# Kernel tuning notes

Hardware: AMD Instinct MI355X
Metric: run time of the kernel (lower is better)

Reference implementation:

```python
import math
import jax, jax.numpy as jnp
from jax import lax
import numpy as np

D_MODEL = 2048
N_HEADS = 16
HEAD_DIM = 128
INNER = N_HEADS * HEAD_DIM  # 2048
KCONV = 4
B, N = 2, 2048


def setup_inputs() -> dict:
    key = jax.random.key(0)
    ks = jax.random.split(key, 7)
    x = jax.random.normal(ks[0], (B, N, D_MODEL), dtype=jnp.float32)
    W_qkv = jax.random.normal(ks[1], (3 * INNER, D_MODEL), dtype=jnp.float32) * 0.02
    conv_w = jax.random.normal(ks[2], (3 * INNER, KCONV), dtype=jnp.float32) * 0.2
    W_ab = jax.random.normal(ks[3], (2 * N_HEADS, D_MODEL), dtype=jnp.float32) * 0.02
    # ab_proj bias init: first H filled with log(0.98/0.02), rest zero
    b_ab = jnp.concatenate([
        jnp.full((N_HEADS,), math.log(0.98 / 0.02), dtype=jnp.float32),
        jnp.zeros((N_HEADS,), dtype=jnp.float32),
    ])
    W_g = jax.random.normal(ks[4], (INNER, D_MODEL), dtype=jnp.float32) * 0.02
    W_o = jax.random.normal(ks[5], (D_MODEL, INNER), dtype=jnp.float32) * 0.02
    return {"x": x, "W_qkv": W_qkv, "conv_w": conv_w, "W_ab": W_ab,
            "b_ab": b_ab, "W_g": W_g, "W_o": W_o}


def _l2_normalize(t, eps=1e-12):
    # torch F.normalize: x / max(||x||_2, eps)
    nrm = jnp.sqrt(jnp.sum(t * t, axis=-1, keepdims=True))
    return t / jnp.maximum(nrm, eps)


def _short_conv(z, conv_w):
    # depthwise causal conv1d + SiLU (FLA-style ShortConvolution, no bias)
    # z: (B, N, C), conv_w: (C, K)
    C, K = conv_w.shape
    zc = jnp.transpose(z, (0, 2, 1))  # (B, C, N)
    kern = conv_w[:, None, :]          # (C, 1, K) -> OIH
    out = lax.conv_general_dilated(
        zc, kern, window_strides=(1,), padding=[(K - 1, 0)],
        dimension_numbers=("NCH", "OIH", "NCH"), feature_group_count=C)
    return jax.nn.silu(jnp.transpose(out, (0, 2, 1)))  # (B, N, C)


def reference(x, W_qkv, conv_w, W_ab, b_ab, W_g, W_o):
    Bq, Nq, _ = x.shape
    H = b_ab.shape[0] // 2
    inner = W_g.shape[0]
    D = inner // H

    qkv = jnp.einsum("bnd,ed->bne", x, W_qkv)            # (B, N, 3*inner)
    qkv = _short_conv(qkv, conv_w)
    q, k, v = jnp.split(qkv, 3, axis=-1)
    to_heads = lambda t: t.reshape(Bq, Nq, H, D).transpose(0, 2, 1, 3)  # (B,H,N,D)
    q, k, v = to_heads(q), to_heads(k), to_heads(v)
    q = _l2_normalize(q)
    k = _l2_normalize(k)

    ab = jnp.einsum("bnd,ed->bne", x, W_ab) + b_ab        # (B, N, 2H)
    alpha = jax.nn.sigmoid(ab[..., :H]).transpose(0, 2, 1)  # (B, H, N)
    beta = jax.nn.sigmoid(ab[..., H:]).transpose(0, 2, 1)   # (B, H, N)

    # gated delta rule recurrence:
    #   S_t = a_t * S_{t-1} + b_t * (v_t - a_t * S_{t-1} k_t) k_t^T
    #   o_t = S_t q_t
    # time-major xs for scan
    q_s = q.transpose(2, 0, 1, 3)   # (N, B, H, D)
    k_s = k.transpose(2, 0, 1, 3)
    v_s = v.transpose(2, 0, 1, 3)
    a_s = alpha.transpose(2, 0, 1)  # (N, B, H)
    b_s = beta.transpose(2, 0, 1)

    S0 = jnp.zeros((Bq, H, D, D), dtype=x.dtype)

    def step(S, inp):
        q_t, k_t, v_t, a_t, b_t = inp
        Sk = jnp.einsum("bhde,bhe->bhd", S, k_t)
        u = b_t[..., None] * (v_t - a_t[..., None] * Sk)
        S = a_t[..., None, None] * S + u[..., :, None] * k_t[..., None, :]
        o = jnp.einsum("bhde,bhe->bhd", S, q_t)
        return S, o

    _, o = lax.scan(step, S0, (q_s, k_s, v_s, a_s, b_s))  # o: (N, B, H, D)
    out = o.transpose(1, 0, 2, 3).reshape(Bq, Nq, inner)

    g = jax.nn.silu(jnp.einsum("bnd,ed->bne", x, W_g))
    out = out * g
    y = jnp.einsum("bne,de->bnd", out, W_o)
    return y
```

## Files before the change

kernel.cpp:

```cpp
#include <hip/hip_runtime.h>
#include <math.h>
#include <stddef.h>

#define B_ 2
#define N_ 2048
#define DM 2048
#define H_ 16
#define HD 128
#define INNER 2048
#define TRIPLE 6144
#define M_ (B_ * N_)
#define T_ 32
#define NCHK (N_ / T_)

typedef __bf16 bf16x8 __attribute__((ext_vector_type(8)));
typedef float  f32x4v __attribute__((ext_vector_type(4)));
typedef __attribute__((address_space(1))) const void gvoid;
typedef __attribute__((address_space(3))) void lvoid;

__device__ __forceinline__ float sig_(float x) { return 1.0f / (1.0f + __expf(-x)); }

__device__ __forceinline__ unsigned short f2bf(float f) {
    unsigned u = __float_as_uint(f);
    u += 0x7FFFu + ((u >> 16) & 1u);
    return (unsigned short)(u >> 16);
}
__device__ __forceinline__ float bf2f(unsigned short h) {
    return __uint_as_float((unsigned)h << 16);
}
__device__ __forceinline__ void unpack8(uint4 r, float* f) {
    f[0] = __uint_as_float(r.x << 16); f[1] = __uint_as_float(r.x & 0xffff0000u);
    f[2] = __uint_as_float(r.y << 16); f[3] = __uint_as_float(r.y & 0xffff0000u);
    f[4] = __uint_as_float(r.z << 16); f[5] = __uint_as_float(r.z & 0xffff0000u);
    f[6] = __uint_as_float(r.w << 16); f[7] = __uint_as_float(r.w & 0xffff0000u);
}

__device__ __forceinline__ void lds_barrier() {
    asm volatile("" ::: "memory");
    __builtin_amdgcn_s_waitcnt(0xC07F);
    __builtin_amdgcn_s_barrier();
    asm volatile("" ::: "memory");
}

__device__ __forceinline__ void bar() {
    asm volatile("" ::: "memory");
    __builtin_amdgcn_s_barrier();
    asm volatile("" ::: "memory");
}

__global__ __launch_bounds__(256) void cast_bf16_3(
    const float* __restrict__ s1, const float* __restrict__ s2,
    const float* __restrict__ s3, unsigned short* __restrict__ dst,
    int n1, int n2, int n3)
{
    int i = (blockIdx.x * 256 + threadIdx.x) * 4;
    const float* s; int off;
    if (i < n1)           { s = s1; off = i; }
    else if (i < n1 + n2) { s = s2; off = i - n1; }
    else if (i < n1 + n2 + n3) { s = s3; off = i - n1 - n2; }
    else return;
    float4 v = *(const float4*)(s + off);
    ushort4 u;
    u.x = f2bf(v.x); u.y = f2bf(v.y); u.z = f2bf(v.z); u.w = f2bf(v.w);
    *(ushort4*)(dst + i) = u;
}

__global__ __launch_bounds__(256) void cast_hilo(
    const float* __restrict__ in, unsigned short* __restrict__ hi,
    unsigned short* __restrict__ lo, int n)
{
    int i = (blockIdx.x * 256 + threadIdx.x) * 4;
    if (i < n) {
        float4 v = *(const float4*)(in + i);
        ushort4 h, l;
        h.x = f2bf(v.x); l.x = f2bf(v.x - bf2f(h.x));
        h.y = f2bf(v.y); l.y = f2bf(v.y - bf2f(h.y));
        h.z = f2bf(v.z); l.z = f2bf(v.z - bf2f(h.z));
        h.w = f2bf(v.w); l.w = f2bf(v.w - bf2f(h.w));
        *(ushort4*)(hi + i) = h;
        *(ushort4*)(lo + i) = l;
    }
}

__global__ __launch_bounds__(512) void gemm_fused256(
    const unsigned short* __restrict__ A, const unsigned short* __restrict__ Bw,
    unsigned short* __restrict__ outQ, float* __restrict__ outG,
    int M, int NQ, int NG, int K)
{
    __shared__ unsigned short As[2][256 * 64];
    __shared__ unsigned short Bs[2][256 * 64];

    const int tid = threadIdx.x;
    const int w   = tid >> 6;
    const int l   = tid & 63;
    const int wm  = w >> 2;
    const int wn  = w & 3;
    const int lr  = l & 15;
    const int kg  = l >> 4;

    const int bid = blockIdx.x;
    const int swz = (bid & 7) * 64 + (bid >> 3);
    const int by  = swz & 15;
    const int bx  = swz >> 4;
    const int row0 = by * 256;
    const int col0 = bx * 256;

    const int srow = w * 8 + (l >> 3);
    const int schk = ((l & 7) ^ (l >> 3)) * 8;
    const unsigned short* Ath = A  + (size_t)(row0 + srow) * K + schk;
    const unsigned short* Bth = Bw + (size_t)(col0 + srow) * K + schk;

    const int fsw0 = ((0 + kg) ^ (lr & 7)) * 8;
    const int fsw1 = ((4 + kg) ^ (lr & 7)) * 8;
    const int arb  = wm * 64 + lr;
    const int brb  = wn * 32 + lr;

    f32x4v acc[2][2][4][2];
#pragma unroll
    for (int a0 = 0; a0 < 2; ++a0)
#pragma unroll
        for (int a1 = 0; a1 < 2; ++a1)
#pragma unroll
            for (int a2 = 0; a2 < 4; ++a2)
#pragma unroll
                for (int a3 = 0; a3 < 2; ++a3)
                    acc[a0][a1][a2][a3] = (f32x4v){0.f, 0.f, 0.f, 0.f};

#define STAGE_A(b, hb, kt) do {                                                  \
        const unsigned short* g_ = Ath + (size_t)((hb) * 128) * K + (kt) * 64;   \
        unsigned short* d_ = &As[b][((hb) * 128 + w * 8) * 64];                  \
        __builtin_amdgcn_global_load_lds((gvoid*)g_, (lvoid*)d_, 16, 0, 0);      \
        __builtin_amdgcn_global_load_lds((gvoid*)(g_ + (size_t)64 * K),          \
                                         (lvoid*)(d_ + 64 * 64), 16, 0, 0);      \
    } while (0)
#define STAGE_B(b, hb, kt) do {                                                  \
        const unsigned short* g_ = Bth + (size_t)((hb) * 128) * K + (kt) * 64;   \
        unsigned short* d_ = &Bs[b][((hb) * 128 + w * 8) * 64];                  \
        __builtin_amdgcn_global_load_lds((gvoid*)g_, (lvoid*)d_, 16, 0, 0);      \
        __builtin_amdgcn_global_load_lds((gvoid*)(g_ + (size_t)64 * K),          \
                                         (lvoid*)(d_ + 64 * 64), 16, 0, 0);      \
    } while (0)

#define RD_A(DST, BASE, HOFF)                                        \
    _Pragma("unroll")                                                \
    for (int m_ = 0; m_ < 4; ++m_) {                                 \
        const int r_ = ((HOFF) + arb + m_ * 16) * 64;                \
        DST[m_][0] = *(const bf16x8*)((BASE) + r_ + fsw0);           \
        DST[m_][1] = *(const bf16x8*)((BASE) + r_ + fsw1);           \
    }
#define RD_B(DST, BASE, HOFF)                                        \
    _Pragma("unroll")                                                \
    for (int n_ = 0; n_ < 2; ++n_) {                                 \
        const int r_ = ((HOFF) + brb + n_ * 16) * 64;                \
        DST[n_][0] = *(const bf16x8*)((BASE) + r_ + fsw0);           \
        DST[n_][1] = *(const bf16x8*)((BASE) + r_ + fsw1);           \
    }
#define Q_MFMA(MH, NH, AF, BF)                                               \
    __builtin_amdgcn_s_setprio(1);                                           \
    _Pragma("unroll")                                                        \
    for (int m_ = 0; m_ < 4; ++m_)                                           \
        _Pragma("unroll")                                                    \
        for (int n_ = 0; n_ < 2; ++n_) {                                     \
            acc[MH][NH][m_][n_] = __builtin_amdgcn_mfma_f32_16x16x32_bf16(   \
                AF[m_][0], BF[n_][0], acc[MH][NH][m_][n_], 0, 0, 0);         \
            acc[MH][NH][m_][n_] = __builtin_amdgcn_mfma_f32_16x16x32_bf16(   \
                AF[m_][1], BF[n_][1], acc[MH][NH][m_][n_], 0, 0, 0);         \
        }                                                                    \
    __builtin_amdgcn_s_setprio(0);

    const int KT = K >> 6;

    STAGE_A(0, 0, 0); STAGE_B(0, 0, 0); STAGE_A(0, 1, 0); STAGE_B(0, 1, 0);
    STAGE_A(1, 0, 1); STAGE_B(1, 1, 1);
    asm volatile("s_waitcnt vmcnt(4)" ::: "memory");
    bar();

    bf16x8 aF[4][2];
    bf16x8 aG[4][2];
    bf16x8 bF0[2][2];
    bf16x8 bF1[2][2];

#pragma unroll 2
    for (int kt = 0; kt < KT; ++kt) {
        const unsigned short* Ab = As[kt & 1];
        const unsigned short* Bb = Bs[kt & 1];
        const int nb = (kt + 1) & 1;

        RD_A(aF, Ab, 0);
        RD_B(bF0, Bb, 0);
        if (kt + 1 < KT) STAGE_B(nb, 0, kt + 1);
        bar();

        Q_MFMA(0, 0, aF, bF0);
        RD_B(bF1, Bb, 128);
        if (kt + 1 < KT) STAGE_A(nb, 1, kt + 1);
        bar();

        Q_MFMA(0, 1, aF, bF1);
        RD_A(aG, Ab, 128);
        if (kt + 2 < KT) STAGE_A(kt & 1, 0, kt + 2);
        bar();

        Q_MFMA(1, 1, aG, bF1);
        if (kt + 2 < KT) STAGE_B(kt & 1, 1, kt + 2);
        if (kt < KT - 2)       { asm volatile("s_waitcnt vmcnt(4)" ::: "memory"); }
        else if (kt == KT - 2) { asm volatile("s_waitcnt vmcnt(0)" ::: "memory"); }
        bar();
        Q_MFMA(1, 0, aG, bF0);
    }
#undef STAGE_A
#undef STAGE_B
#undef RD_A
#undef RD_B
#undef Q_MFMA

    const bool isG = (col0 >= NQ);
#pragma unroll
    for (int mh = 0; mh < 2; ++mh)
#pragma unroll
    for (int m = 0; m < 4; ++m) {
        const int rbase = row0 + mh * 128 + wm * 64 + m * 16 + kg * 4;
#pragma unroll
        for (int nh = 0; nh < 2; ++nh)
#pragma unroll
        for (int n = 0; n < 2; ++n) {
            const int c = col0 + nh * 128 + wn * 32 + n * 16 + lr;
#pragma unroll
            for (int j = 0; j < 4; ++j) {
                float v = acc[mh][nh][m][n][j];
                const size_t r = (size_t)(rbase + j);
                if (!isG) {
                    outQ[r * NQ + c] = f2bf(v);
                } else {
                    v = v * sig_(v);
                    outG[r * NG + (c - NQ)] = v;
                }
            }
        }
    }
}

__global__ __launch_bounds__(256) void gemm_bf16f(
    const unsigned short* __restrict__ A, const unsigned short* __restrict__ Bw,
    float* __restrict__ C, int M, int N, int K)
{
    __shared__ unsigned short As[2][128 * 64];
    __shared__ unsigned short Bs[2][128 * 64];

    const int tid = threadIdx.x;
    const int w   = tid >> 6;
    const int l   = tid & 63;
    const int wm  = w >> 1;
    const int wn  = w & 1;
    const int lr  = l & 15;
    const int kg  = l >> 4;

    const int bid = blockIdx.x;
    const int swz = (bid & 7) * 64 + (bid >> 3);
    const int by  = swz & 31;
    const int bx  = swz >> 5;
    const int row0 = by * 128;
    const int col0 = bx * 128;

    const int srow = w * 8 + (l >> 3);
    const int schk = ((l & 7) ^ (l >> 3)) * 8;
    const unsigned short* Ath = A  + (size_t)(row0 + srow) * K + schk;
    const unsigned short* Bth = Bw + (size_t)(col0 + srow) * K + schk;

    const int fsw0 = ((0 + kg) ^ (lr & 7)) * 8;
    const int fsw1 = ((4 + kg) ^ (lr & 7)) * 8;
    const int arb  = wm * 64 + lr;
    const int brb  = wn * 64 + lr;

    f32x4v acc[4][4];
#pragma unroll
    for (int i = 0; i < 4; ++i)
#pragma unroll
        for (int j = 0; j < 4; ++j) acc[i][j] = (f32x4v){0.f, 0.f, 0.f, 0.f};

#define STAGE_T(buf, kt) do {                                                    \
        _Pragma("unroll")                                                        \
        for (int p_ = 0; p_ < 4; ++p_) {                                         \
            const unsigned short* ga_ = Ath + (size_t)(p_ * 32) * K + (kt) * 64; \
            const unsigned short* gb_ = Bth + (size_t)(p_ * 32) * K + (kt) * 64; \
            unsigned short* da_ = &As[buf][(p_ * 32 + w * 8) * 64];              \
            unsigned short* db_ = &Bs[buf][(p_ * 32 + w * 8) * 64];              \
            __builtin_amdgcn_global_load_lds((gvoid*)ga_, (lvoid*)da_, 16, 0, 0);\
            __builtin_amdgcn_global_load_lds((gvoid*)gb_, (lvoid*)db_, 16, 0, 0);\
        }                                                                        \
    } while (0)

    const int KT = K >> 6;

    STAGE_T(0, 0);
    STAGE_T(1, 1);
    asm volatile("s_waitcnt vmcnt(8)" ::: "memory");
    bar();

    bf16x8 aF[4][2], bF[4][2];

#pragma unroll 2
    for (int kt = 0; kt < KT; ++kt) {
        const unsigned short* Ab = As[kt & 1];
        const unsigned short* Bb = Bs[kt & 1];

#pragma unroll
        for (int m_ = 0; m_ < 4; ++m_) {
            const int r_ = (arb + m_ * 16) * 64;
            aF[m_][0] = *(const bf16x8*)(Ab + r_ + fsw0);
            aF[m_][1] = *(const bf16x8*)(Ab + r_ + fsw1);
        }
#pragma unroll
        for (int n_ = 0; n_ < 4; ++n_) {
            const int r_ = (brb + n_ * 16) * 64;
            bF[n_][0] = *(const bf16x8*)(Bb + r_ + fsw0);
            bF[n_][1] = *(const bf16x8*)(Bb + r_ + fsw1);
        }
        bar();

        if (kt + 2 < KT) STAGE_T(kt & 1, kt + 2);

        __builtin_amdgcn_s_setprio(1);
#pragma unroll
        for (int ks = 0; ks < 2; ++ks)
#pragma unroll
            for (int m_ = 0; m_ < 4; ++m_)
#pragma unroll
                for (int n_ = 0; n_ < 4; ++n_)
                    acc[m_][n_] = __builtin_amdgcn_mfma_f32_16x16x32_bf16(
                        aF[m_][ks], bF[n_][ks], acc[m_][n_], 0, 0, 0);
        __builtin_amdgcn_s_setprio(0);

        if (kt < KT - 2) {
            asm volatile("s_waitcnt vmcnt(8)" ::: "memory");
        } else if (kt == KT - 2) {
            asm volatile("s_waitcnt vmcnt(0)" ::: "memory");
        }
        bar();
    }
#undef STAGE_T

#pragma unroll
    for (int m_ = 0; m_ < 4; ++m_)
#pragma unroll
        for (int j = 0; j < 4; ++j) {
            const int r = row0 + wm * 64 + m_ * 16 + kg * 4 + j;
#pragma unroll
            for (int n_ = 0; n_ < 4; ++n_) {
                const int c = col0 + wn * 64 + n_ * 16 + lr;
                C[(size_t)r * N + c] = acc[m_][n_][j];
            }
        }
}

__global__ __launch_bounds__(256) void gemm_ab(
    const unsigned short* __restrict__ xhi, const unsigned short* __restrict__ xlo,
    const unsigned short* __restrict__ wh, const unsigned short* __restrict__ wl,
    const float* __restrict__ b_ab, float* __restrict__ absig)
{
    __shared__ float sums[4][16][32];
    const int tid = threadIdx.x;
    const int w = tid >> 6, lane = tid & 63;
    const int lr = lane & 15, lk8 = (lane >> 4) * 8, lrow4 = (lane >> 4) * 4;
    const int row = blockIdx.x * 16 + lr;
    const int kw  = w * (DM / 4);

    f32x4v acc[2];
    acc[0] = (f32x4v){0.f,0.f,0.f,0.f};
    acc[1] = (f32x4v){0.f,0.f,0.f,0.f};
    const unsigned short* Ah = xhi + (size_t)row * DM + kw;
    const unsigned short* Al = xlo + (size_t)row * DM + kw;

    for (int k0 = 0; k0 < DM / 4; k0 += 32) {
        bf16x8 ah = *(const bf16x8*)(Ah + k0 + lk8);
        bf16x8 al = *(const bf16x8*)(Al + k0 + lk8);
#pragma unroll
        for (int nt = 0; nt < 2; ++nt) {
            bf16x8 whf = *(const bf16x8*)(wh + (size_t)(nt * 16 + lr) * DM + kw + k0 + lk8);
            bf16x8 wlf = *(const bf16x8*)(wl + (size_t)(nt * 16 + lr) * DM + kw + k0 + lk8);
            acc[nt] = __builtin_amdgcn_mfma_f32_16x16x32_bf16(ah, whf, acc[nt], 0, 0, 0);
            acc[nt] = __builtin_amdgcn_mfma_f32_16x16x32_bf16(ah, wlf, acc[nt], 0, 0, 0);
            acc[nt] = __builtin_amdgcn_mfma_f32_16x16x32_bf16(al, whf, acc[nt], 0, 0, 0);
        }
    }

#pragma unroll
    for (int nt = 0; nt < 2; ++nt)
#pragma unroll
        for (int j = 0; j < 4; ++j)
            sums[w][lrow4 + j][nt * 16 + lr] = acc[nt][j];
    __syncthreads();

// ... 210 lines not shown
        const size_t cb = (size_t)bh * NCHK;
        const unsigned short* Am = Ab + (size_t)(mt * 16 + lr) * TRIPLE;
#pragma unroll
        for (int ks = 0; ks < 4; ++ks) aF[ks] = *(const bf16x8*)(Am + ks * 32 + lk8);
        if (!isQ) {
            wmF = *(const bf16x8*)(What + cb * (T_*T_) + (mt * 16 + lr) * T_ + lk8);
#pragma unroll
            for (int j = 0; j < 4; ++j)
                sc4[j] = Ubar[cb * (T_*HD) + (mt * 16 + lrow4 + j) * HD + d0 + lr];
        } else {
            wmF = *(const bf16x8*)(Mhat + cb * (T_*T_) + (mt * 16 + lr) * T_ + lk8);
#pragma unroll
            for (int j = 0; j < 4; ++j) {
                sc4[j] = Pbuf[cb * T_ + mt * 16 + lrow4 + j];
                g4[j]  = gb[(size_t)(mt * 16 + lrow4 + j) * INNER + d0 + lr];
            }
        }
#pragma unroll
        for (int j2 = 0; j2 < 2; ++j2)
            khF[j2] = *(const bf16x8*)(KhatT + cb * (HD*T_) + ((2*w + j2) * 16 + lr) * T_ + lk8);
        gam = Pbuf[cb * T_ + T_ - 1];
    }
    __syncthreads();

    for (int c = 0; c < NCHK; ++c) {
        const int np = (c + 1 < NCHK) ? c + 1 : c;
        const size_t cbn = (size_t)bh * NCHK + np;
        const int tok0n = np * T_;
        bf16x8 aFn[4], wmFn, khFn[2];
        float sc4n[4], g4n[4], gamn;
        {
            const unsigned short* Am = Ab + (size_t)(tok0n + mt * 16 + lr) * TRIPLE;
#pragma unroll
            for (int ks = 0; ks < 4; ++ks) aFn[ks] = *(const bf16x8*)(Am + ks * 32 + lk8);
            if (!isQ) {
                wmFn = *(const bf16x8*)(What + cbn * (T_*T_) + (mt * 16 + lr) * T_ + lk8);
#pragma unroll
                for (int j = 0; j < 4; ++j)
                    sc4n[j] = Ubar[cbn * (T_*HD) + (mt * 16 + lrow4 + j) * HD + d0 + lr];
            } else {
                wmFn = *(const bf16x8*)(Mhat + cbn * (T_*T_) + (mt * 16 + lr) * T_ + lk8);
#pragma unroll
                for (int j = 0; j < 4; ++j) {
                    sc4n[j] = Pbuf[cbn * T_ + mt * 16 + lrow4 + j];
                    g4n[j]  = gb[(size_t)(tok0n + mt * 16 + lrow4 + j) * INNER + d0 + lr];
                }
            }
#pragma unroll
            for (int j2 = 0; j2 < 2; ++j2)
                khFn[j2] = *(const bf16x8*)(KhatT + cbn * (HD*T_) + ((2*w + j2) * 16 + lr) * T_ + lk8);
            gamn = Pbuf[cbn * T_ + T_ - 1];
        }

        f32x4v accH = {0.f,0.f,0.f,0.f}, accL = {0.f,0.f,0.f,0.f};
#pragma unroll
        for (int ks = 0; ks < 4; ++ks) {
            bf16x8 hi = *(const bf16x8*)&Shi[lr * 136 + ks * 32 + lk8];
            bf16x8 lo = *(const bf16x8*)&Slo[lr * 136 + ks * 32 + lk8];
            accH = __builtin_amdgcn_mfma_f32_16x16x32_bf16(aF[ks], hi, accH, 0, 0, 0);
            accL = __builtin_amdgcn_mfma_f32_16x16x32_bf16(aF[ks], lo, accL, 0, 0, 0);
        }
        f32x4v accB;
#pragma unroll
        for (int j = 0; j < 4; ++j) accB[j] = accH[j] + accL[j];

        if (!isQ) {
            ushort4 cv;
            cv.x = f2bf(-accB[0]); cv.y = f2bf(-accB[1]);
            cv.z = f2bf(-accB[2]); cv.w = f2bf(-accB[3]);
            *(ushort4*)&CT[lr * 40 + mt * 16 + lrow4] = cv;
        }
        lds_barrier();

        if (!isQ) {
            f32x4v accU;
#pragma unroll
            for (int j = 0; j < 4; ++j) accU[j] = sc4[j];
            bf16x8 bC = *(const bf16x8*)&CT[lr * 40 + lk8];
            accU = __builtin_amdgcn_mfma_f32_16x16x32_bf16(wmF, bC, accU, 0, 0, 0);
            ushort4 uv;
            uv.x = f2bf(accU[0]); uv.y = f2bf(accU[1]);
            uv.z = f2bf(accU[2]); uv.w = f2bf(accU[3]);
            *(ushort4*)&UT[lr * 40 + mt * 16 + lrow4] = uv;
        }
        lds_barrier();

        bf16x8 utF = *(const bf16x8*)&UT[lr * 40 + lk8];

        if (isQ) {
            f32x4v accO;
#pragma unroll
            for (int j = 0; j < 4; ++j) accO[j] = sc4[j] * accB[j];
            accO = __builtin_amdgcn_mfma_f32_16x16x32_bf16(wmF, utF, accO, 0, 0, 0);
            const int tokb = c * T_ + mt * 16 + lrow4;
#pragma unroll
            for (int j = 0; j < 4; ++j)
                ogb[(size_t)(tokb + j) * INNER + d0 + lr] = f2bf(accO[j] * g4[j]);
        }

#pragma unroll
        for (int j2 = 0; j2 < 2; ++j2) {
            const int et = 2 * w + j2;
            f32x4v accS;
#pragma unroll
            for (int j = 0; j < 4; ++j)
                accS[j] = gam * S[(lrow4 + j) * 132 + et * 16 + lr];
            accS = __builtin_amdgcn_mfma_f32_16x16x32_bf16(utF, khF[j2], accS, 0, 0, 0);
#pragma unroll
            for (int j = 0; j < 4; ++j) {
                float v = accS[j];
                S[(lrow4 + j) * 132 + et * 16 + lr] = v;
                unsigned short hh = f2bf(v);
                Shi[(lrow4 + j) * 136 + et * 16 + lr] = hh;
                Slo[(lrow4 + j) * 136 + et * 16 + lr] = f2bf(v - bf2f(hh));
            }
        }
        lds_barrier();

#pragma unroll
        for (int ks = 0; ks < 4; ++ks) aF[ks] = aFn[ks];
        wmF = wmFn;
#pragma unroll
        for (int j = 0; j < 4; ++j) { sc4[j] = sc4n[j]; g4[j] = g4n[j]; }
        khF[0] = khFn[0]; khF[1] = khFn[1];
        gam = gamn;
    }
}

extern "C" void kernel_launch(void* const* d_in, const int* in_sizes, int n_in,
                              void* d_out, int out_size, void* d_ws, size_t ws_size,
                              hipStream_t stream) {
    const float* x      = (const float*)d_in[0];
    const float* W_qkv  = (const float*)d_in[1];
    const float* conv_w = (const float*)d_in[2];
    const float* W_ab   = (const float*)d_in[3];
    const float* b_ab   = (const float*)d_in[4];
    const float* W_g    = (const float*)d_in[5];
    const float* W_o    = (const float*)d_in[6];
    float* out = (float*)d_out;

    char* p = (char*)d_ws;
    unsigned short* wqkvb   = (unsigned short*)p; p += (size_t)TRIPLE * DM * 2;
    unsigned short* wgb     = (unsigned short*)p; p += (size_t)INNER * DM * 2;
    unsigned short* wob     = (unsigned short*)p; p += (size_t)DM * INNER * 2;
    unsigned short* wabhi   = (unsigned short*)p; p += (size_t)32 * DM * 2;
    unsigned short* wablo   = (unsigned short*)p; p += (size_t)32 * DM * 2;
    unsigned short* xb      = (unsigned short*)p; p += (size_t)M_ * DM * 2;
    unsigned short* xlo     = (unsigned short*)p; p += (size_t)M_ * DM * 2;
    unsigned short* qkv_pre = (unsigned short*)p; p += (size_t)M_ * TRIPLE * 2;
    unsigned short* qkv_c   = (unsigned short*)p; p += (size_t)M_ * TRIPLE * 2;
    float*          absig   = (float*)p;          p += (size_t)M_ * 32 * 4;
    float*          gpre    = (float*)p;          p += (size_t)M_ * INNER * 4;
    unsigned short* ogb     = (unsigned short*)p; p += (size_t)M_ * INNER * 2;

    char* q = (char*)xb;
    float*          Ubar  = (float*)q;          q += (size_t)32 * NCHK * T_ * HD * 4;
    unsigned short* KhatT = (unsigned short*)q; q += (size_t)32 * NCHK * HD * T_ * 2;
    unsigned short* What  = (unsigned short*)q; q += (size_t)32 * NCHK * T_ * T_ * 2;
    unsigned short* Mhat  = (unsigned short*)q; q += (size_t)32 * NCHK * T_ * T_ * 2;
    float*          Pbuf  = (float*)q;          q += (size_t)32 * NCHK * T_ * 4;

    dim3 blk(256);
    cast_hilo<<<dim3((M_ * DM) / 1024), blk, 0, stream>>>(x, xb, xlo, M_ * DM);
    cast_bf16_3<<<dim3((TRIPLE * DM + INNER * DM + DM * INNER) / 1024), blk, 0, stream>>>(
        W_qkv, W_g, W_o, wqkvb, TRIPLE * DM, INNER * DM, DM * INNER);
    cast_hilo<<<dim3((32 * DM) / 1024), blk, 0, stream>>>(W_ab, wabhi, wablo, 32 * DM);

    gemm_fused256<<<dim3(((TRIPLE + INNER) / 256) * (M_ / 256)), dim3(512), 0, stream>>>(
        xb, wqkvb, qkv_pre, gpre, M_, TRIPLE, INNER, DM);
    gemm_ab<<<dim3(M_ / 16), blk, 0, stream>>>(xb, xlo, wabhi, wablo, b_ab, absig);
    conv_silu_norm<<<dim3(B_ * N_), blk, 0, stream>>>(qkv_pre, conv_w, qkv_c);

    chunk_prep<<<dim3(32 * NCHK), blk, 0, stream>>>(qkv_c, absig, Ubar, What, Mhat, KhatT, Pbuf);
    chunk_scan<<<dim3(256), blk, 0, stream>>>(qkv_c, gpre, Ubar, What, Mhat, KhatT, Pbuf, ogb);

    gemm_bf16f<<<dim3((M_ / 128) * (INNER / 128)), blk, 0, stream>>>(
        ogb, wob, out, M_, INNER, DM);
}
```

Measured before the change: 556.1 us.

## Pre-pack weights into MFMA fragment layout and load B directly to registers

The QKV+gate weights are cast to bf16 in a packed layout of 16x32 fragments, so each lane of the fused GEMM can load its B operand straight from global memory into registers with contiguous 16-byte reads. This removes the B tile from LDS, which halves shared memory use and drops two of the four barriers per k-tile. The main loop is rewritten as a register double-buffered two-step body, with A still staged through LDS. It trades LDS traffic and syncs for more global load latency on the critical path and extra register pressure. The W_o cast becomes a separate kernel with scalar stores.

```diff
diff --git a/kernel.cpp b/kernel.cpp
--- a/kernel.cpp
+++ b/kernel.cpp
@@ -48,21 +48,35 @@
     asm volatile("" ::: "memory");
 }
 
-__global__ __launch_bounds__(256) void cast_bf16_3(
-    const float* __restrict__ s1, const float* __restrict__ s2,
-    const float* __restrict__ s3, unsigned short* __restrict__ dst,
-    int n1, int n2, int n3)
+__global__ __launch_bounds__(256) void cast_bf16(
+    const float* __restrict__ in, unsigned short* __restrict__ out, int n)
 {
     int i = (blockIdx.x * 256 + threadIdx.x) * 4;
-    const float* s; int off;
-    if (i < n1)           { s = s1; off = i; }
-    else if (i < n1 + n2) { s = s2; off = i - n1; }
-    else if (i < n1 + n2 + n3) { s = s3; off = i - n1 - n2; }
-    else return;
-    float4 v = *(const float4*)(s + off);
-    ushort4 u;
-    u.x = f2bf(v.x); u.y = f2bf(v.y); u.z = f2bf(v.z); u.w = f2bf(v.w);
-    *(ushort4*)(dst + i) = u;
+    if (i < n) {
+        float4 v = *(const float4*)(in + i);
+        out[i + 0] = f2bf(v.x); out[i + 1] = f2bf(v.y);
+        out[i + 2] = f2bf(v.z); out[i + 3] = f2bf(v.w);
+    }
+}
+
+__global__ __launch_bounds__(256) void pack_cast_w(
+    const float* __restrict__ Wq, const float* __restrict__ Wg,
+    unsigned short* __restrict__ dst)
+{
+    const int i = blockIdx.x * 256 + threadIdx.x;
+    const int e = i * 8;
+    const int n = e >> 11;
+    const int k = e & 2047;
+    const float* src = (n < TRIPLE) ? (Wq + (size_t)n * DM + k)
+                                    : (Wg + (size_t)(n - TRIPLE) * DM + k);
+    float4 v0 = *(const float4*)(src);
+    float4 v1 = *(const float4*)(src + 4);
+    ushort4 u0, u1;
+    u0.x = f2bf(v0.x); u0.y = f2bf(v0.y); u0.z = f2bf(v0.z); u0.w = f2bf(v0.w);
+    u1.x = f2bf(v1.x); u1.y = f2bf(v1.y); u1.z = f2bf(v1.z); u1.w = f2bf(v1.w);
+    const size_t off = ((size_t)((n >> 4) * 64 + (k >> 5)) << 9) + (n & 15) * 32 + (k & 31);
+    *(ushort4*)(dst + off)     = u0;
+    *(ushort4*)(dst + off + 4) = u1;
 }
 
 __global__ __launch_bounds__(256) void cast_hilo(
@@ -83,12 +97,11 @@
 }
 
 __global__ __launch_bounds__(512) void gemm_fused256(
-    const unsigned short* __restrict__ A, const unsigned short* __restrict__ Bw,
+    const unsigned short* __restrict__ A, const unsigned short* __restrict__ Bp,
     unsigned short* __restrict__ outQ, float* __restrict__ outG,
     int M, int NQ, int NG, int K)
 {
     __shared__ unsigned short As[2][256 * 64];
-    __shared__ unsigned short Bs[2][256 * 64];
 
     const int tid = threadIdx.x;
     const int w   = tid >> 6;
@@ -107,13 +120,19 @@
 
     const int srow = w * 8 + (l >> 3);
     const int schk = ((l & 7) ^ (l >> 3)) * 8;
-    const unsigned short* Ath = A  + (size_t)(row0 + srow) * K + schk;
-    const unsigned short* Bth = Bw + (size_t)(col0 + srow) * K + schk;
+    const unsigned short* Ath = A + (size_t)(row0 + srow) * K + schk;
 
     const int fsw0 = ((0 + kg) ^ (lr & 7)) * 8;
     const int fsw1 = ((4 + kg) ^ (lr & 7)) * 8;
     const int arb  = wm * 64 + lr;
-    const int brb  = wn * 32 + lr;
+
+    const unsigned short* Bl0 = Bp + lr * 32 + kg * 8;
+    int nbOff[2][2];
+#pragma unroll
+    for (int nh_ = 0; nh_ < 2; ++nh_)
+#pragma unroll
+        for (int n_ = 0; n_ < 2; ++n_)
+            nbOff[nh_][n_] = (((col0 >> 4) + nh_ * 8 + wn * 2 + n_) << 15);
 
     f32x4v acc[2][2][4][2];
 #pragma unroll
@@ -126,19 +145,24 @@
                 for (int a3 = 0; a3 < 2; ++a3)
                     acc[a0][a1][a2][a3] = (f32x4v){0.f, 0.f, 0.f, 0.f};
 
-#define STAGE_A(b, hb, kt) do {                                                  \
-        const unsigned short* g_ = Ath + (size_t)((hb) * 128) * K + (kt) * 64;   \
-        unsigned short* d_ = &As[b][((hb) * 128 + w * 8) * 64];                  \
-        __builtin_amdgcn_global_load_lds((gvoid*)g_, (lvoid*)d_, 16, 0, 0);      \
-        __builtin_amdgcn_global_load_lds((gvoid*)(g_ + (size_t)64 * K),          \
-                                         (lvoid*)(d_ + 64 * 64), 16, 0, 0);      \
+#define STAGE_T(buf, kt) do {                                                    \
+        _Pragma("unroll")                                                        \
+        for (int p_ = 0; p_ < 4; ++p_) {                                         \
+            const unsigned short* g_ = Ath + (size_t)(p_ * 64) * K + (kt) * 64;  \
+            unsigned short* d_ = &As[buf][(p_ * 64 + w * 8) * 64];               \
+            __builtin_amdgcn_global_load_lds((gvoid*)g_, (lvoid*)d_, 16, 0, 0);  \
+        }                                                                        \
     } while (0)
-#define STAGE_B(b, hb, kt) do {                                                  \
-        const unsigned short* g_ = Bth + (size_t)((hb) * 128) * K + (kt) * 64;   \
-        unsigned short* d_ = &Bs[b][((hb) * 128 + w * 8) * 64];                  \
-        __builtin_amdgcn_global_load_lds((gvoid*)g_, (lvoid*)d_, 16, 0, 0);      \
-        __builtin_amdgcn_global_load_lds((gvoid*)(g_ + (size_t)64 * K),          \
-                                         (lvoid*)(d_ + 64 * 64), 16, 0, 0);      \
+
+#define LOAD_B(DST, kt) do {                                                     \
+        _Pragma("unroll")                                                        \
+        for (int nh_ = 0; nh_ < 2; ++nh_)                                        \
+        _Pragma("unroll")                                                        \
+        for (int n_ = 0; n_ < 2; ++n_)                                           \
+        _Pragma("unroll")                                                        \
+        for (int ks_ = 0; ks_ < 2; ++ks_)                                        \
+            DST[nh_][n_][ks_] = *(const bf16x8*)(                                \
+                Bl0 + nbOff[nh_][n_] + ((kt) * 2 + ks_) * 512);                  \
     } while (0)
 
 #define RD_A(DST, BASE, HOFF)                                        \
@@ -148,70 +172,59 @@
         DST[m_][0] = *(const bf16x8*)((BASE) + r_ + fsw0);           \
         DST[m_][1] = *(const bf16x8*)((BASE) + r_ + fsw1);           \
     }
-#define RD_B(DST, BASE, HOFF)                                        \
-    _Pragma("unroll")                                                \
-    for (int n_ = 0; n_ < 2; ++n_) {                                 \
-        const int r_ = ((HOFF) + brb + n_ * 16) * 64;                \
-        DST[n_][0] = *(const bf16x8*)((BASE) + r_ + fsw0);           \
-        DST[n_][1] = *(const bf16x8*)((BASE) + r_ + fsw1);           \
-    }
-#define Q_MFMA(MH, NH, AF, BF)                                               \
+
+#define Q_MFMA(MH, NH, AF, BB)                                               \
     __builtin_amdgcn_s_setprio(1);                                           \
     _Pragma("unroll")                                                        \
     for (int m_ = 0; m_ < 4; ++m_)                                           \
         _Pragma("unroll")                                                    \
         for (int n_ = 0; n_ < 2; ++n_) {                                     \
             acc[MH][NH][m_][n_] = __builtin_amdgcn_mfma_f32_16x16x32_bf16(   \
-                AF[m_][0], BF[n_][0], acc[MH][NH][m_][n_], 0, 0, 0);         \
+                AF[m_][0], BB[NH][n_][0], acc[MH][NH][m_][n_], 0, 0, 0);     \
             acc[MH][NH][m_][n_] = __builtin_amdgcn_mfma_f32_16x16x32_bf16(   \
-                AF[m_][1], BF[n_][1], acc[MH][NH][m_][n_], 0, 0, 0);         \
+                AF[m_][1], BB[NH][n_][1], acc[MH][NH][m_][n_], 0, 0, 0);     \
         }                                                                    \
     __builtin_amdgcn_s_setprio(0);
 
     const int KT = K >> 6;
 
-    STAGE_A(0, 0, 0); STAGE_B(0, 0, 0); STAGE_A(0, 1, 0); STAGE_B(0, 1, 0);
-    STAGE_A(1, 0, 1); STAGE_B(1, 1, 1);
-    asm volatile("s_waitcnt vmcnt(4)" ::: "memory");
+    bf16x8 aF[4][2], aG[4][2];
+    bf16x8 bX[2][2][2], bY[2][2][2];
+
+    STAGE_T(0, 0);
+    STAGE_T(1, 1);
+    LOAD_B(bX, 0);
+    asm volatile("s_waitcnt vmcnt(12)" ::: "memory");
     bar();
 
-    bf16x8 aF[4][2];
-    bf16x8 aG[4][2];
-    bf16x8 bF0[2][2];
-    bf16x8 bF1[2][2];
-
-#pragma unroll 2
-    for (int kt = 0; kt < KT; ++kt) {
-        const unsigned short* Ab = As[kt & 1];
-        const unsigned short* Bb = Bs[kt & 1];
-        const int nb = (kt + 1) & 1;
-
-        RD_A(aF, Ab, 0);
-        RD_B(bF0, Bb, 0);
-        if (kt + 1 < KT) STAGE_B(nb, 0, kt + 1);
-        bar();
-
-        Q_MFMA(0, 0, aF, bF0);
-        RD_B(bF1, Bb, 128);
-        if (kt + 1 < KT) STAGE_A(nb, 1, kt + 1);
-        bar();
-
-        Q_MFMA(0, 1, aF, bF1);
-        RD_A(aG, Ab, 128);
-        if (kt + 2 < KT) STAGE_A(kt & 1, 0, kt + 2);
-        bar();
-
-        Q_MFMA(1, 1, aG, bF1);
-        if (kt + 2 < KT) STAGE_B(kt & 1, 1, kt + 2);
-        if (kt < KT - 2)       { asm volatile("s_waitcnt vmcnt(4)" ::: "memory"); }
-        else if (kt == KT - 2) { asm volatile("s_waitcnt vmcnt(0)" ::: "memory"); }
-        bar();
-        Q_MFMA(1, 0, aG, bF0);
-    }
-#undef STAGE_A
-#undef STAGE_B
+#define TILE_BODY(kt, BCUR, BNXT) do {                                          \
+        const unsigned short* Ab = As[(kt) & 1];                                \
+        RD_A(aF, Ab, 0);                                                        \
+        if ((kt) + 1 < KT) LOAD_B(BNXT, (kt) + 1);                              \
+        Q_MFMA(0, 0, aF, BCUR);                                                 \
+        Q_MFMA(0, 1, aF, BCUR);                                                 \
+        RD_A(aG, Ab, 128);                                                      \
+        Q_MFMA(1, 1, aG, BCUR);                                                 \
+        Q_MFMA(1, 0, aG, BCUR);                                                 \
+        if ((kt) + 2 < KT) {                                                    \
+            bar();                             \
+            STAGE_T((kt) & 1, (kt) + 2);                                        \
+        }                                                                       \
+        if ((kt) + 1 < KT) {                                                    \
+            if ((kt) < KT - 2) { asm volatile("s_waitcnt vmcnt(12)" ::: "memory"); } \
+            else               { asm volatile("s_waitcnt vmcnt(8)"  ::: "memory"); } \
+            bar();                                  \
+        }                                                                       \
+    } while (0)
+
+    for (int kt = 0; kt < KT; kt += 2) {
+        TILE_BODY(kt,     bX, bY);
+        TILE_BODY(kt + 1, bY, bX);
+    }
+#undef TILE_BODY
+#undef STAGE_T
+#undef LOAD_B
 #undef RD_A
-#undef RD_B
 #undef Q_MFMA
 
     const bool isG = (col0 >= NQ);
@@ -754,6 +767,7 @@
     float*          absig   = (float*)p;          p += (size_t)M_ * 32 * 4;
     float*          gpre    = (float*)p;          p += (size_t)M_ * INNER * 4;
     unsigned short* ogb     = (unsigned short*)p; p += (size_t)M_ * INNER * 2;
+    (void)wgb;
 
     char* q = (char*)xb;
     float*          Ubar  = (float*)q;          q += (size_t)32 * NCHK * T_ * HD * 4;
@@ -764,8 +778,9 @@
 
     dim3 blk(256);
     cast_hilo<<<dim3((M_ * DM) / 1024), blk, 0, stream>>>(x, xb, xlo, M_ * DM);
-    cast_bf16_3<<<dim3((TRIPLE * DM + INNER * DM + DM * INNER) / 1024), blk, 0, stream>>>(
-        W_qkv, W_g, W_o, wqkvb, TRIPLE * DM, INNER * DM, DM * INNER);
+    pack_cast_w<<<dim3(((TRIPLE + INNER) * DM / 8) / 256), blk, 0, stream>>>(
+        W_qkv, W_g, wqkvb);
+    cast_bf16<<<dim3((INNER * DM) / 1024), blk, 0, stream>>>(W_o, wob, INNER * DM);
     cast_hilo<<<dim3((32 * DM) / 1024), blk, 0, stream>>>(W_ab, wabhi, wablo, 32 * DM);
 
     gemm_fused256<<<dim3(((TRIPLE + INNER) / 256) * (M_ / 256)), dim3(512), 0, stream>>>(
```

Result: slower. 585.0 us (+5.2%).

## Switch fused QKV/gate GEMM to 128x128 tiles and merge cast kernels

Applied to the files above, without the earlier changes.

Replaces the 256x256, 512-thread fused projection GEMM with a 128x128, 256-thread version that uses a simpler two-stage global-to-LDS double buffer. This gives four times as many blocks and less LDS per block, and folds the three fp32-to-bf16 cast launches into one kernel. The aim is better occupancy and load balance across CUs and fewer launches. In exchange, each block reuses less data, which raises global/L2 traffic per FLOP.

```diff
diff --git a/kernel.cpp b/kernel.cpp
--- a/kernel.cpp
+++ b/kernel.cpp
@@ -48,62 +48,72 @@
     asm volatile("" ::: "memory");
 }
 
-__global__ __launch_bounds__(256) void cast_bf16_3(
-    const float* __restrict__ s1, const float* __restrict__ s2,
-    const float* __restrict__ s3, unsigned short* __restrict__ dst,
-    int n1, int n2, int n3)
+#define NX_ (M_ * DM)
+#define NW_ ((TRIPLE + 2 * INNER) * DM)
+#define NAB_ (32 * DM)
+__global__ __launch_bounds__(256) void cast_all(
+    const float* __restrict__ x, const float* __restrict__ Wq,
+    const float* __restrict__ Wg, const float* __restrict__ Wo,
+    const float* __restrict__ Wab,
+    unsigned short* __restrict__ xb, unsigned short* __restrict__ xlo,
+    unsigned short* __restrict__ wfused,
+    unsigned short* __restrict__ wabhi, unsigned short* __restrict__ wablo)
 {
-    int i = (blockIdx.x * 256 + threadIdx.x) * 4;
-    const float* s; int off;
-    if (i < n1)           { s = s1; off = i; }
-    else if (i < n1 + n2) { s = s2; off = i - n1; }
-    else if (i < n1 + n2 + n3) { s = s3; off = i - n1 - n2; }
-    else return;
-    float4 v = *(const float4*)(s + off);
-    ushort4 u;
-    u.x = f2bf(v.x); u.y = f2bf(v.y); u.z = f2bf(v.z); u.w = f2bf(v.w);
-    *(ushort4*)(dst + i) = u;
-}
-
-__global__ __launch_bounds__(256) void cast_hilo(
-    const float* __restrict__ in, unsigned short* __restrict__ hi,
-    unsigned short* __restrict__ lo, int n)
-{
-    int i = (blockIdx.x * 256 + threadIdx.x) * 4;
-    if (i < n) {
-        float4 v = *(const float4*)(in + i);
+    const int i = (blockIdx.x * 256 + threadIdx.x) * 4;
+    if (i < NX_) {
+        float4 v = *(const float4*)(x + i);
         ushort4 h, l;
         h.x = f2bf(v.x); l.x = f2bf(v.x - bf2f(h.x));
         h.y = f2bf(v.y); l.y = f2bf(v.y - bf2f(h.y));
         h.z = f2bf(v.z); l.z = f2bf(v.z - bf2f(h.z));
         h.w = f2bf(v.w); l.w = f2bf(v.w - bf2f(h.w));
-        *(ushort4*)(hi + i) = h;
-        *(ushort4*)(lo + i) = l;
-    }
-}
-
-__global__ __launch_bounds__(512) void gemm_fused256(
+        *(ushort4*)(xb + i)  = h;
+        *(ushort4*)(xlo + i) = l;
+    } else if (i < NX_ + NW_) {
+        const int j = i - NX_;
+        const float* s;
+        if (j < TRIPLE * DM)                s = Wq + j;
+        else if (j < (TRIPLE + INNER) * DM) s = Wg + (j - TRIPLE * DM);
+        else                                s = Wo + (j - (TRIPLE + INNER) * DM);
+        float4 v = *(const float4*)s;
+        ushort4 u;
+        u.x = f2bf(v.x); u.y = f2bf(v.y); u.z = f2bf(v.z); u.w = f2bf(v.w);
+        *(ushort4*)(wfused + j) = u;
+    } else if (i < NX_ + NW_ + NAB_) {
+        const int j = i - NX_ - NW_;
+        float4 v = *(const float4*)(Wab + j);
+        ushort4 h, l;
+        h.x = f2bf(v.x); l.x = f2bf(v.x - bf2f(h.x));
+        h.y = f2bf(v.y); l.y = f2bf(v.y - bf2f(h.y));
+        h.z = f2bf(v.z); l.z = f2bf(v.z - bf2f(h.z));
+        h.w = f2bf(v.w); l.w = f2bf(v.w - bf2f(h.w));
+        *(ushort4*)(wabhi + j) = h;
+        *(ushort4*)(wablo + j) = l;
+    }
+}
+
+__global__ __launch_bounds__(256) void gemm_fused128(
     const unsigned short* __restrict__ A, const unsigned short* __restrict__ Bw,
     unsigned short* __restrict__ outQ, float* __restrict__ outG,
     int M, int NQ, int NG, int K)
 {
-    __shared__ unsigned short As[2][256 * 64];
-    __shared__ unsigned short Bs[2][256 * 64];
+    __shared__ unsigned short As[2][128 * 64];
+    __shared__ unsigned short Bs[2][128 * 64];
 
     const int tid = threadIdx.x;
     const int w   = tid >> 6;
     const int l   = tid & 63;
-    const int wm  = w >> 2;
-    const int wn  = w & 3;
+    const int wm  = w >> 1;
+    const int wn  = w & 1;
     const int lr  = l & 15;
     const int kg  = l >> 4;
 
     const int bid = blockIdx.x;
-    const int swz = (bid & 7) * 64 + (bid >> 3);
-    const int by  = swz & 15;
-    const int bx  = swz >> 4;
-    const int row0 = by * 256;
-    const int col0 = bx * 256;
+    const int swz = (bid & 7) * 256 + (bid >> 3);
+    const int by  = swz & 31;
+    const int bx  = swz >> 5;
+    const int row0 = by * 128;
+    const int col0 = bx * 128;
 
     const int srow = w * 8 + (l >> 3);
     const int schk = ((l & 7) ^ (l >> 3)) * 8;
@@ -113,131 +123,94 @@
     const int fsw0 = ((0 + kg) ^ (lr & 7)) * 8;
     const int fsw1 = ((4 + kg) ^ (lr & 7)) * 8;
     const int arb  = wm * 64 + lr;
-    const int brb  = wn * 32 + lr;
-
-    f32x4v acc[2][2][4][2];
-#pragma unroll
-    for (int a0 = 0; a0 < 2; ++a0)
-#pragma unroll
-        for (int a1 = 0; a1 < 2; ++a1)
-#pragma unroll
-            for (int a2 = 0; a2 < 4; ++a2)
-#pragma unroll
-                for (int a3 = 0; a3 < 2; ++a3)
-                    acc[a0][a1][a2][a3] = (f32x4v){0.f, 0.f, 0.f, 0.f};
-
-#define STAGE_A(b, hb, kt) do {                                                  \
-        const unsigned short* g_ = Ath + (size_t)((hb) * 128) * K + (kt) * 64;   \
-        unsigned short* d_ = &As[b][((hb) * 128 + w * 8) * 64];                  \
-        __builtin_amdgcn_global_load_lds((gvoid*)g_, (lvoid*)d_, 16, 0, 0);      \
-        __builtin_amdgcn_global_load_lds((gvoid*)(g_ + (size_t)64 * K),          \
-                                         (lvoid*)(d_ + 64 * 64), 16, 0, 0);      \
+    const int brb  = wn * 64 + lr;
+
+    f32x4v acc[4][4];
+#pragma unroll
+    for (int i = 0; i < 4; ++i)
+#pragma unroll
+        for (int j = 0; j < 4; ++j) acc[i][j] = (f32x4v){0.f, 0.f, 0.f, 0.f};
+
+#define STAGE_F(buf, kt) do {                                                    \
+        _Pragma("unroll")                                                        \
+        for (int p_ = 0; p_ < 4; ++p_) {                                         \
+            const unsigned short* ga_ = Ath + (size_t)(p_ * 32) * K + (kt) * 64; \
+            const unsigned short* gb_ = Bth + (size_t)(p_ * 32) * K + (kt) * 64; \
+            unsigned short* da_ = &As[buf][(p_ * 32 + w * 8) * 64];              \
+            unsigned short* db_ = &Bs[buf][(p_ * 32 + w * 8) * 64];              \
+            __builtin_amdgcn_global_load_lds((gvoid*)ga_, (lvoid*)da_, 16, 0, 0);\
+            __builtin_amdgcn_global_load_lds((gvoid*)gb_, (lvoid*)db_, 16, 0, 0);\
+        }                                                                        \
     } while (0)
-#define STAGE_B(b, hb, kt) do {                                                  \
-        const unsigned short* g_ = Bth + (size_t)((hb) * 128) * K + (kt) * 64;   \
-        unsigned short* d_ = &Bs[b][((hb) * 128 + w * 8) * 64];                  \
-        __builtin_amdgcn_global_load_lds((gvoid*)g_, (lvoid*)d_, 16, 0, 0);      \
-        __builtin_amdgcn_global_load_lds((gvoid*)(g_ + (size_t)64 * K),          \
-                                         (lvoid*)(d_ + 64 * 64), 16, 0, 0);      \
-    } while (0)
-
-#define RD_A(DST, BASE, HOFF)                                        \
-    _Pragma("unroll")                                                \
-    for (int m_ = 0; m_ < 4; ++m_) {                                 \
-        const int r_ = ((HOFF) + arb + m_ * 16) * 64;                \
-        DST[m_][0] = *(const bf16x8*)((BASE) + r_ + fsw0);           \
-        DST[m_][1] = *(const bf16x8*)((BASE) + r_ + fsw1);           \
-    }
-#define RD_B(DST, BASE, HOFF)                                        \
-    _Pragma("unroll")                                                \
-    for (int n_ = 0; n_ < 2; ++n_) {                                 \
-        const int r_ = ((HOFF) + brb + n_ * 16) * 64;                \
-        DST[n_][0] = *(const bf16x8*)((BASE) + r_ + fsw0);           \
-        DST[n_][1] = *(const bf16x8*)((BASE) + r_ + fsw1);           \
-    }
-#define Q_MFMA(MH, NH, AF, BF)                                               \
-    __builtin_amdgcn_s_setprio(1);                                           \
-    _Pragma("unroll")                                                        \
-    for (int m_ = 0; m_ < 4; ++m_)                                           \
-        _Pragma("unroll")                                                    \
-        for (int n_ = 0; n_ < 2; ++n_) {                                     \
-            acc[MH][NH][m_][n_] = __builtin_amdgcn_mfma_f32_16x16x32_bf16(   \
-                AF[m_][0], BF[n_][0], acc[MH][NH][m_][n_], 0, 0, 0);         \
-            acc[MH][NH][m_][n_] = __builtin_amdgcn_mfma_f32_16x16x32_bf16(   \
-                AF[m_][1], BF[n_][1], acc[MH][NH][m_][n_], 0, 0, 0);         \
-        }                                                                    \
-    __builtin_amdgcn_s_setprio(0);
 
     const int KT = K >> 6;
 
-    STAGE_A(0, 0, 0); STAGE_B(0, 0, 0); STAGE_A(0, 1, 0); STAGE_B(0, 1, 0);
-    STAGE_A(1, 0, 1); STAGE_B(1, 1, 1);
-    asm volatile("s_waitcnt vmcnt(4)" ::: "memory");
+    STAGE_F(0, 0);
+    STAGE_F(1, 1);
+    asm volatile("s_waitcnt vmcnt(8)" ::: "memory");
     bar();
 
-    bf16x8 aF[4][2];
-    bf16x8 aG[4][2];
-    bf16x8 bF0[2][2];
-    bf16x8 bF1[2][2];
+    bf16x8 aF[4][2], bF[4][2];
 
 #pragma unroll 2
     for (int kt = 0; kt < KT; ++kt) {
         const unsigned short* Ab = As[kt & 1];
         const unsigned short* Bb = Bs[kt & 1];
-        const int nb = (kt + 1) & 1;
-
-        RD_A(aF, Ab, 0);
-        RD_B(bF0, Bb, 0);
-        if (kt + 1 < KT) STAGE_B(nb, 0, kt + 1);
+
+#pragma unroll
+        for (int m_ = 0; m_ < 4; ++m_) {
+            const int r_ = (arb + m_ * 16) * 64;
+            aF[m_][0] = *(const bf16x8*)(Ab + r_ + fsw0);
+            aF[m_][1] = *(const bf16x8*)(Ab + r_ + fsw1);
+        }
+#pragma unroll
+        for (int n_ = 0; n_ < 4; ++n_) {
+            const int r_ = (brb + n_ * 16) * 64;
+            bF[n_][0] = *(const bf16x8*)(Bb + r_ + fsw0);
+            bF[n_][1] = *(const bf16x8*)(Bb + r_ + fsw1);
+        }
         bar();
 
-        Q_MFMA(0, 0, aF, bF0);
-        RD_B(bF1, Bb, 128);
-        if (kt + 1 < KT) STAGE_A(nb, 1, kt + 1);
+        if (kt + 2 < KT) STAGE_F(kt & 1, kt + 2);
+
+        __builtin_amdgcn_s_setprio(1);
+#pragma unroll
+        for (int ks = 0; ks < 2; ++ks)
+#pragma unroll
+            for (int m_ = 0; m_ < 4; ++m_)
+#pragma unroll
+                for (int n_ = 0; n_ < 4; ++n_)
+                    acc[m_][n_] = __builtin_amdgcn_mfma_f32_16x16x32_bf16(
+                        aF[m_][ks], bF[n_][ks], acc[m_][n_], 0, 0, 0);
+        __builtin_amdgcn_s_setprio(0);
+
+        if (kt < KT - 2) {
+            asm volatile("s_waitcnt vmcnt(8)" ::: "memory");
+        } else if (kt == KT - 2) {
+            asm volatile("s_waitcnt vmcnt(0)" ::: "memory");
+        }
         bar();
-
-        Q_MFMA(0, 1, aF, bF1);
-        RD_A(aG, Ab, 128);
-        if (kt + 2 < KT) STAGE_A(kt & 1, 0, kt + 2);
-        bar();
-
-        Q_MFMA(1, 1, aG, bF1);
-        if (kt + 2 < KT) STAGE_B(kt & 1, 1, kt + 2);
-        if (kt < KT - 2)       { asm volatile("s_waitcnt vmcnt(4)" ::: "memory"); }
-        else if (kt == KT - 2) { asm volatile("s_waitcnt vmcnt(0)" ::: "memory"); }
-        bar();
-        Q_MFMA(1, 0, aG, bF0);
-    }
-#undef STAGE_A
-#undef STAGE_B
-#undef RD_A
-#undef RD_B
-#undef Q_MFMA
+    }
+#undef STAGE_F
 
     const bool isG = (col0 >= NQ);
 #pragma unroll
-    for (int mh = 0; mh < 2; ++mh)
-#pragma unroll
-    for (int m = 0; m < 4; ++m) {
-        const int rbase = row0 + mh * 128 + wm * 64 + m * 16 + kg * 4;
-#pragma unroll
-        for (int nh = 0; nh < 2; ++nh)
-#pragma unroll
-        for (int n = 0; n < 2; ++n) {
-            const int c = col0 + nh * 128 + wn * 32 + n * 16 + lr;
-#pragma unroll
-            for (int j = 0; j < 4; ++j) {
-                float v = acc[mh][nh][m][n][j];
-                const size_t r = (size_t)(rbase + j);
+    for (int m_ = 0; m_ < 4; ++m_)
+#pragma unroll
+        for (int j = 0; j < 4; ++j) {
+            const int r = row0 + wm * 64 + m_ * 16 + kg * 4 + j;
+#pragma unroll
+            for (int n_ = 0; n_ < 4; ++n_) {
+                const int c = col0 + wn * 64 + n_ * 16 + lr;
+                float v = acc[m_][n_][j];
                 if (!isG) {
-                    outQ[r * NQ + c] = f2bf(v);
+                    outQ[(size_t)r * NQ + c] = f2bf(v);
                 } else {
                     v = v * sig_(v);
-                    outG[r * NG + (c - NQ)] = v;
+                    outG[(size_t)r * NG + (c - NQ)] = v;
                 }
             }
         }
-    }
 }
 
 __global__ __launch_bounds__(256) void gemm_bf16f(
@@ -754,6 +727,7 @@
     float*          absig   = (float*)p;          p += (size_t)M_ * 32 * 4;
     float*          gpre    = (float*)p;          p += (size_t)M_ * INNER * 4;
     unsigned short* ogb     = (unsigned short*)p; p += (size_t)M_ * INNER * 2;
+    (void)wgb;
 
     char* q = (char*)xb;
     float*          Ubar  = (float*)q;          q += (size_t)32 * NCHK * T_ * HD * 4;
@@ -763,12 +737,10 @@
     float*          Pbuf  = (float*)q;          q += (size_t)32 * NCHK * T_ * 4;
 
     dim3 blk(256);
-    cast_hilo<<<dim3((M_ * DM) / 1024), blk, 0, stream>>>(x, xb, xlo, M_ * DM);
-    cast_bf16_3<<<dim3((TRIPLE * DM + INNER * DM + DM * INNER) / 1024), blk, 0, stream>>>(
-        W_qkv, W_g, W_o, wqkvb, TRIPLE * DM, INNER * DM, DM * INNER);
-    cast_hilo<<<dim3((32 * DM) / 1024), blk, 0, stream>>>(W_ab, wabhi, wablo, 32 * DM);
-
-    gemm_fused256<<<dim3(((TRIPLE + INNER) / 256) * (M_ / 256)), dim3(512), 0, stream>>>(
+    cast_all<<<dim3((NX_ + NW_ + NAB_) / 1024), blk, 0, stream>>>(
+        x, W_qkv, W_g, W_o, W_ab, xb, xlo, wqkvb, wabhi, wablo);
+
+    gemm_fused128<<<dim3((M_ / 128) * ((TRIPLE + INNER) / 128)), blk, 0, stream>>>(
         xb, wqkvb, qkv_pre, gpre, M_, TRIPLE, INNER, DM);
     gemm_ab<<<dim3(M_ / 16), blk, 0, stream>>>(xb, xlo, wabhi, wablo, b_ab, absig);
     conv_silu_norm<<<dim3(B_ * N_), blk, 0, stream>>>(qkv_pre, conv_w, qkv_c);
```

Result: slower. 580.7 us (+4.4%).
